# Kernel tuning notes

Hardware: AMD Instinct MI355X
Metric: run time of the kernel (lower is better)

Reference implementation:

```python
import jax, jax.numpy as jnp
import numpy as np

N = 50000          # nodes
H = 202            # hidden = text(200) + selector(2)
E = 100000         # edges per forward edge type
FWD_TYPES = 3      # forward edge types; backward doubles to 6
LAYER_TIMESTEPS = (2,)
POS_MAX = 1024


def _pos_table():
    # transformer-style sinusoidal embeddings for positions [0, POS_MAX)
    inv_freq = 1.0 / (10000.0 ** (jnp.arange(0, H, 2, dtype=jnp.float32) / H))  # [H/2]
    pos = jnp.arange(POS_MAX, dtype=jnp.float32)
    sinusoid = pos[:, None] * inv_freq[None, :]                                  # [POS_MAX, H/2]
    return jnp.concatenate([jnp.sin(sinusoid), jnp.cos(sinusoid)], axis=-1)      # [POS_MAX, H]


def setup_inputs() -> dict:
    key = jax.random.key(0)
    ks = jax.random.split(key, 11)
    L = len(LAYER_TIMESTEPS)
    s = 0.1
    return {
        "node_states": jax.random.normal(ks[0], (N, H), jnp.float32),
        "edge_lists": jax.random.randint(ks[1], (FWD_TYPES, E, 2), 0, N, jnp.int32),
        "pos_lists": jax.random.randint(ks[2], (FWD_TYPES, E), 0, POS_MAX, jnp.int32),
        "msg_W": jax.random.normal(ks[3], (L, H, 2 * FWD_TYPES * H), jnp.float32) * s,
        "msg_b": jax.random.normal(ks[4], (L, 2 * FWD_TYPES * H), jnp.float32) * s,
        "pos_W": jax.random.normal(ks[5], (L, H, H), jnp.float32) * s,
        "pos_b": jax.random.normal(ks[6], (L, H), jnp.float32) * s,
        "gru_Wih": jax.random.normal(ks[7], (L, 3 * H, H), jnp.float32) * s,
        "gru_Whh": jax.random.normal(ks[8], (L, 3 * H, H), jnp.float32) * s,
        "gru_bih": jax.random.normal(ks[9], (L, 3 * H), jnp.float32) * s,
        "gru_bhh": jax.random.normal(ks[10], (L, 3 * H), jnp.float32) * s,
    }


def _ggnn(node_states, src, tgt, pos, divisor,
          msg_W, msg_b, pos_W, pos_b, gru_Wih, gru_Whh, gru_bih, gru_bhh):
    ET = src.shape[0]  # 2 * FWD_TYPES edge types (forward + backward)
    h = node_states
    pos_table = _pos_table()
    for l, steps in enumerate(LAYER_TIMESTEPS):
        # 2*sigmoid(pos_transform(position_embs)) gating, per position id
        gate = 2.0 * jax.nn.sigmoid(pos_table @ pos_W[l] + pos_b[l])  # [POS_MAX, H]
        for _ in range(steps):
            # fused per-edge-type transforms: [N, ET*H] chunked -> [N, ET, H]
            prop = (h @ msg_W[l] + msg_b[l]).reshape(h.shape[0], ET, H)
            messages = jnp.zeros_like(h)
            for i in range(ET):  # small fixed loop over edge types
                m = prop[:, i, :][src[i]] * gate[pos[i]]  # [E, H]
                messages = messages.at[tgt[i]].add(m)
            messages = messages / divisor  # mean aggregation
            # nn.GRUCell(messages, h)
            gi = messages @ gru_Wih[l].T + gru_bih[l]
            gh = h @ gru_Whh[l].T + gru_bhh[l]
            ir, iz, inn = jnp.split(gi, 3, axis=1)
            hr, hz, hn = jnp.split(gh, 3, axis=1)
            r = jax.nn.sigmoid(ir + hr)
            z = jax.nn.sigmoid(iz + hz)
            n = jnp.tanh(inn + r * hn)
            h = (1.0 - z) * n + z * h
    return h


def reference(node_states, edge_lists, pos_lists, msg_W, msg_b, pos_W, pos_b,
              gru_Wih, gru_Whh, gru_bih, gru_bhh):
    # backward edges = flipped forward edges; pos lists duplicated
    src = jnp.concatenate([edge_lists[:, :, 0], edge_lists[:, :, 1]], axis=0)  # [6, E]
    tgt = jnp.concatenate([edge_lists[:, :, 1], edge_lists[:, :, 0]], axis=0)  # [6, E]
    pos = jnp.clip(jnp.concatenate([pos_lists, pos_lists], axis=0), 0, POS_MAX - 1)
    # target bincount over all edge types; zero counts -> 1
    counts = jnp.zeros((node_states.shape[0],), jnp.float32).at[tgt.reshape(-1)].add(1.0)
    divisor = jnp.where(counts == 0, 1.0, counts)[:, None]
    out = _ggnn(node_states, src, tgt, pos, divisor, msg_W, msg_b, pos_W, pos_b,
                gru_Wih, gru_Whh, gru_bih, gru_bhh)
    return out, node_states
```

## Files before the change

### kernel.cpp

```cpp
#include <hip/hip_runtime.h>

#define NN 50000
#define HH 202
#define EE 100000
#define PMX 1024
#define NKT 7
#define PKS2 (16 * NKT * 64 * 8)
#define NEDG (6 * EE)
#define AFR (4 * NKT * 64 * 8)

typedef __attribute__((ext_vector_type(8))) short short8;
typedef __attribute__((ext_vector_type(4))) float v4f;

__device__ __forceinline__ float sigf(float x) { return 1.0f / (1.0f + expf(-x)); }

__device__ __forceinline__ unsigned short f2bf(float x) {
    unsigned int u = __float_as_uint(x);
    unsigned int r = (u + 0x7fffu + ((u >> 16) & 1u)) >> 16;
    return (unsigned short)r;
}
__device__ __forceinline__ float bf2f(unsigned short u) {
    return __uint_as_float(((unsigned int)u) << 16);
}
__device__ __forceinline__ float bflo(unsigned int u) {
    return __uint_as_float(u << 16);
}
__device__ __forceinline__ float bfhi(unsigned int u) {
    return __uint_as_float(u & 0xffff0000u);
}
__device__ __forceinline__ unsigned int bfpack(float lo, float hi) {
    return (unsigned int)f2bf(lo) | ((unsigned int)f2bf(hi) << 16);
}

__global__ void gate_kernel(const float* __restrict__ pos_W, const float* __restrict__ pos_b,
                            unsigned short* __restrict__ gate) {
    int p = blockIdx.x;
    __shared__ float pt[HH];
    int t = threadIdx.x;
    if (t < HH) {
        float v;
        if (t < 101) {
            float invf = expf(-(2.0f * t / 202.0f) * 9.210340371976184f);
            v = sinf((float)p * invf);
        } else {
            int k = t - 101;
            float invf = expf(-(2.0f * k / 202.0f) * 9.210340371976184f);
            v = cosf((float)p * invf);
        }
        pt[t] = v;
    }
    __syncthreads();
    for (int j = t; j < HH; j += blockDim.x) {
        float acc = pos_b[j];
        for (int k = 0; k < HH; ++k) acc += pt[k] * pos_W[k * HH + j];
        gate[p * HH + j] = f2bf(2.0f * sigf(acc));
    }
}

__global__ void pack_kernel(const float* __restrict__ S, int ldb, int row0, int col0, int mode,
                            unsigned short* __restrict__ BP) {
    int idx = blockIdx.x * blockDim.x + threadIdx.x;
    if (idx >= PKS2) return;
    int jj = idx & 7;
    int l = (idx >> 3) & 63;
    int r2 = idx >> 9;
    int cf = r2 / NKT, kt = r2 - cf * NKT;
    int k = kt * 32 + ((l >> 4) << 3) + jj;
    int j = cf * 16 + (l & 15);
    float v = 0.0f;
    if (k < HH && j < HH)
        v = mode ? S[(size_t)(row0 + j) * HH + k] : S[(size_t)k * ldb + col0 + j];
    BP[idx] = f2bf(v);
}

__global__ void count_kernel(const int* __restrict__ el, int* __restrict__ cnt) {
    int idx = blockIdx.x * blockDim.x + threadIdx.x;
    if (idx >= NEDG) return;
    int ty = idx / EE, e = idx - ty * EE;
    int2 pr = (ty < 3) ? reinterpret_cast<const int2*>(el)[ty * EE + e]
                       : reinterpret_cast<const int2*>(el)[(ty - 3) * EE + e];
    int tg = (ty < 3) ? pr.y : pr.x;
    atomicAdd(&cnt[tg], 1);
}

__global__ void scan1_kernel(const int* __restrict__ cnt, int* __restrict__ off,
                             int* __restrict__ bsum) {
    __shared__ int sd[256];
    int t = threadIdx.x, i = blockIdx.x * 256 + t;
    int v = (i < NN) ? cnt[i] : 0;
    sd[t] = v;
    __syncthreads();
    for (int s = 1; s < 256; s <<= 1) {
        int u = (t >= s) ? sd[t - s] : 0;
        __syncthreads();
        sd[t] += u;
        __syncthreads();
    }
    if (i < NN) off[i] = sd[t] - v;
    if (t == 255) bsum[blockIdx.x] = sd[255];
}

__global__ void scan2_kernel(int* __restrict__ bsum, int nb) {
    __shared__ int sd[256];
    int t = threadIdx.x;
    int v = (t < nb) ? bsum[t] : 0;
    sd[t] = v;
    __syncthreads();
    for (int s = 1; s < 256; s <<= 1) {
        int u = (t >= s) ? sd[t - s] : 0;
        __syncthreads();
        sd[t] += u;
        __syncthreads();
    }
    if (t < nb) bsum[t] = sd[t] - v;
}

__global__ void scan3_kernel(int* __restrict__ off, const int* __restrict__ bsum,
                             int* __restrict__ cursor) {
    int i = blockIdx.x * 256 + threadIdx.x;
    if (i < NN) {
        int o = off[i] + bsum[blockIdx.x];
        off[i] = o;
        cursor[i] = o;
    }
    if (i == 0) off[NN] = NEDG;
}

__global__ void inv_kernel(const int* __restrict__ cnt, float* __restrict__ inv) {
    int n = blockIdx.x * blockDim.x + threadIdx.x;
    if (n < NN) inv[n] = 1.0f / (float)max(cnt[n], 1);
}

__global__ void fill_kernel(const int* __restrict__ el, const int* __restrict__ pl,
                            int* __restrict__ cursor, int* __restrict__ edg) {
    int idx = blockIdx.x * blockDim.x + threadIdx.x;
    if (idx >= NEDG) return;
    int ty = idx / EE, e = idx - ty * EE;
    int s, tg;
    if (ty < 3) {
        int2 pr = reinterpret_cast<const int2*>(el)[ty * EE + e];
        s = pr.x; tg = pr.y;
    } else {
        int2 pr = reinterpret_cast<const int2*>(el)[(ty - 3) * EE + e];
        s = pr.y; tg = pr.x;
    }
    int p = pl[(ty % 3) * EE + e];
    p = min(max(p, 0), PMX - 1);
    int slot = atomicAdd(&cursor[tg], 1);
    edg[slot] = (s << 13) | (ty << 10) | p;
}

__device__ __forceinline__ int frag_off(int row, int k) {
    return (((row >> 4) * NKT + (k >> 5)) * 64 + ((k >> 3) & 3) * 16 + (row & 15)) * 8 + (k & 7);
}

__global__ __launch_bounds__(512, 4) void gemm9(
    const void* __restrict__ Asrc, int a_is_f32,
    const unsigned short* __restrict__ BPbase, int npack,
    const float* __restrict__ bias,
    unsigned short* __restrict__ O0, unsigned short* __restrict__ O1, int split) {
    __shared__ alignas(16) unsigned short a_lds[AFR];
    __shared__ alignas(16) unsigned short c_lds[64 * HH];
    const int t = threadIdx.x;
    const int w = t >> 6;
    const int l = t & 63;
    const int lm = l & 15, lh = l >> 4;
    const int rowg = w >> 2, colg = w & 3;
    const int cs = colg * 4;
    const int base = blockIdx.x * 64;
    const int vrows = min(64, NN - base);
    const int nu4 = (vrows * 101) >> 2;

    if (a_is_f32) {
        const float* A = (const float*)Asrc;
        for (int idx = t; idx < 64 * 101; idx += 512) {
            int row = idx / 101;
            int c = idx - row * 101;
            int gn = base + row;
            float2 v = make_float2(0.f, 0.f);
            if (gn < NN) v = *reinterpret_cast<const float2*>(&A[(size_t)gn * HH + c * 2]);
            ushort2 bv; bv.x = f2bf(v.x); bv.y = f2bf(v.y);
            *reinterpret_cast<ushort2*>(&a_lds[frag_off(row, c * 2)]) = bv;
        }
    } else {
        const unsigned short* A = (const unsigned short*)Asrc;
        for (int idx = t; idx < 64 * 101; idx += 512) {
            int row = idx / 101;
            int c = idx - row * 101;
            int gn = base + row;
            ushort2 v; v.x = 0; v.y = 0;
            if (gn < NN) v = *reinterpret_cast<const ushort2*>(&A[(size_t)gn * HH + c * 2]);
            *reinterpret_cast<ushort2*>(&a_lds[frag_off(row, c * 2)]) = v;
        }
    }
    for (int idx = t; idx < 64 * 11; idx += 512) {
        int row = idx / 11;
        int c = idx - row * 11;
        ushort2 z; z.x = 0; z.y = 0;
        *reinterpret_cast<ushort2*>(&a_lds[frag_off(row, HH + c * 2)]) = z;
    }
    __syncthreads();

    const int aoff0 = (rowg * 2) * (NKT * 512) + l * 8;
    const int aoff1 = aoff0 + NKT * 512;

#pragma unroll 1
    for (int p = 0; p < npack; ++p) {
        const unsigned short* BP = BPbase + (size_t)p * PKS2 + (size_t)l * 8;
        const unsigned short* Bs0 = BP + (size_t)(cs + 0) * (NKT * 512);
        const unsigned short* Bs1 = BP + (size_t)(cs + 1) * (NKT * 512);
        const unsigned short* Bs2 = BP + (size_t)(cs + 2) * (NKT * 512);
        const unsigned short* Bs3 = BP + (size_t)(cs + 3) * (NKT * 512);

        v4f acc[4][2];
#pragma unroll
        for (int ci = 0; ci < 4; ++ci) {
            acc[ci][0] = (v4f){0.f, 0.f, 0.f, 0.f};
            acc[ci][1] = (v4f){0.f, 0.f, 0.f, 0.f};
        }

        short8 bA0 = *reinterpret_cast<const short8*>(Bs0);
        short8 bA1 = *reinterpret_cast<const short8*>(Bs1);
        short8 bA2 = *reinterpret_cast<const short8*>(Bs2);
        short8 bA3 = *reinterpret_cast<const short8*>(Bs3);
        short8 bB0 = *reinterpret_cast<const short8*>(Bs0 + 512);
        short8 bB1 = *reinterpret_cast<const short8*>(Bs1 + 512);
        short8 bB2 = *reinterpret_cast<const short8*>(Bs2 + 512);
        short8 bB3 = *reinterpret_cast<const short8*>(Bs3 + 512);
        short8 ac0 = *reinterpret_cast<const short8*>(&a_lds[aoff0]);
        short8 ac1 = *reinterpret_cast<const short8*>(&a_lds[aoff1]);

#pragma unroll
        for (int kt = 0; kt < NKT; ++kt) {
            const int k2 = (kt + 2 <= 6) ? (kt + 2) : 6;
            const int ka2 = k2 * 512;
            short8 bC0 = *reinterpret_cast<const short8*>(Bs0 + ka2);
            short8 bC1 = *reinterpret_cast<const short8*>(Bs1 + ka2);
            short8 bC2 = *reinterpret_cast<const short8*>(Bs2 + ka2);
            short8 bC3 = *reinterpret_cast<const short8*>(Bs3 + ka2);
            const int kn = (kt + 1 <= 6) ? (kt + 1) : 6;
            short8 an0 = *reinterpret_cast<const short8*>(&a_lds[aoff0 + kn * 512]);
            short8 an1 = *reinterpret_cast<const short8*>(&a_lds[aoff1 + kn * 512]);

            acc[0][0] = __builtin_amdgcn_mfma_f32_16x16x32_bf16(ac0, bA0, acc[0][0], 0, 0, 0);
            acc[0][1] = __builtin_amdgcn_mfma_f32_16x16x32_bf16(ac1, bA0, acc[0][1], 0, 0, 0);
            acc[1][0] = __builtin_amdgcn_mfma_f32_16x16x32_bf16(ac0, bA1, acc[1][0], 0, 0, 0);
            acc[1][1] = __builtin_amdgcn_mfma_f32_16x16x32_bf16(ac1, bA1, acc[1][1], 0, 0, 0);
            acc[2][0] = __builtin_amdgcn_mfma_f32_16x16x32_bf16(ac0, bA2, acc[2][0], 0, 0, 0);
            acc[2][1] = __builtin_amdgcn_mfma_f32_16x16x32_bf16(ac1, bA2, acc[2][1], 0, 0, 0);
            acc[3][0] = __builtin_amdgcn_mfma_f32_16x16x32_bf16(ac0, bA3, acc[3][0], 0, 0, 0);
            acc[3][1] = __builtin_amdgcn_mfma_f32_16x16x32_bf16(ac1, bA3, acc[3][1], 0, 0, 0);

            ac0 = an0; ac1 = an1;
            bA0 = bB0; bA1 = bB1; bA2 = bB2; bA3 = bB3;
            bB0 = bC0; bB1 = bC1; bB2 = bC2; bB3 = bC3;
        }

        __syncthreads();
#pragma unroll
        for (int ci = 0; ci < 4; ++ci) {
            int col = (cs + ci) * 16 + lm;
            if (col < HH) {
                float bb = bias ? bias[p * HH + col] : 0.0f;
#pragma unroll
                for (int rfi = 0; rfi < 2; ++rfi) {
#pragma unroll
                    for (int r = 0; r < 4; ++r)
                        c_lds[(rowg * 32 + rfi * 16 + lh * 4 + r) * HH + col] =
                            f2bf(acc[ci][rfi][r] + bb);
                }
            }
        }
        __syncthreads();

        unsigned short* slab = (p < split) ? O0 + (size_t)p * NN * HH
                                           : O1 + (size_t)(p - split) * NN * HH;
        uint4* dst = reinterpret_cast<uint4*>(slab + (size_t)base * HH);
        const uint4* srcp = reinterpret_cast<const uint4*>(c_lds);
        for (int i = t; i < nu4; i += 512) dst[i] = srcp[i];
    }
}

__global__ void agg_kernel(const unsigned short* __restrict__ CH0,
                           const unsigned short* __restrict__ CH45,
                           const int* __restrict__ off, const int* __restrict__ edg,
                           const unsigned short* __restrict__ gate,
                           const float* __restrict__ inv, unsigned short* __restrict__ msgb) {
    int n = blockIdx.x * 4 + (threadIdx.x >> 6);
    if (n >= NN) return;
    int lane = threadIdx.x & 63;
    int s0 = off[n], s1 = off[n + 1];
    const int u1 = 64 + lane;
    const bool u1ok = u1 < 101;
    float a0 = 0.f, a1 = 0.f, a2 = 0.f, a3 = 0.f;
    float b0 = 0.f, b1 = 0.f, b2 = 0.f, b3 = 0.f;
    int i = s0;
    for (; i + 1 < s1; i += 2) {
        int recA = edg[i], recB = edg[i + 1];
        int sA = recA >> 13, tyA = (recA >> 10) & 7, pA = recA & 1023;
        int sB = recB >> 13, tyB = (recB >> 10) & 7, pB = recB & 1023;
        const unsigned int* crA = reinterpret_cast<const unsigned int*>(
            ((tyA < 4) ? CH0 + (size_t)tyA * NN * HH : CH45 + (size_t)(tyA - 4) * NN * HH)
            + (size_t)sA * HH);
        const unsigned int* crB = reinterpret_cast<const unsigned int*>(
            ((tyB < 4) ? CH0 + (size_t)tyB * NN * HH : CH45 + (size_t)(tyB - 4) * NN * HH)
            + (size_t)sB * HH);
        const unsigned int* grA = reinterpret_cast<const unsigned int*>(gate + (size_t)pA * HH);
        const unsigned int* grB = reinterpret_cast<const unsigned int*>(gate + (size_t)pB * HH);
        unsigned int cA0 = crA[lane], gA0 = grA[lane];
        unsigned int cB0 = crB[lane], gB0 = grB[lane];
        a0 += bflo(cA0) * bflo(gA0);
        a1 += bfhi(cA0) * bfhi(gA0);
        b0 += bflo(cB0) * bflo(gB0);
        b1 += bfhi(cB0) * bfhi(gB0);
        if (u1ok) {
            unsigned int cA1 = crA[u1], gA1 = grA[u1];
            unsigned int cB1 = crB[u1], gB1 = grB[u1];
            a2 += bflo(cA1) * bflo(gA1);
            a3 += bfhi(cA1) * bfhi(gA1);
            b2 += bflo(cB1) * bflo(gB1);
            b3 += bfhi(cB1) * bfhi(gB1);
        }
    }
    if (i < s1) {
        int rec = edg[i];
        int src = rec >> 13, ty = (rec >> 10) & 7, p = rec & 1023;
        const unsigned int* cr = reinterpret_cast<const unsigned int*>(
            ((ty < 4) ? CH0 + (size_t)ty * NN * HH : CH45 + (size_t)(ty - 4) * NN * HH)
            + (size_t)src * HH);
        const unsigned int* gr = reinterpret_cast<const unsigned int*>(gate + (size_t)p * HH);
        unsigned int c0 = cr[lane], g0 = gr[lane];
        a0 += bflo(c0) * bflo(g0);
        a1 += bfhi(c0) * bfhi(g0);
        if (u1ok) {
            unsigned int c1 = cr[u1], g1 = gr[u1];
            a2 += bflo(c1) * bflo(g1);
            a3 += bfhi(c1) * bfhi(g1);
        }
    }
    float iv = inv[n];
    unsigned int* mr = reinterpret_cast<unsigned int*>(msgb + (size_t)n * HH);
    mr[lane] = bfpack((a0 + b0) * iv, (a1 + b1) * iv);
    if (u1ok) mr[u1] = bfpack((a2 + b2) * iv, (a3 + b3) * iv);
}

__global__ void gru_ew(float* __restrict__ h, const float* __restrict__ hsrc,
                       const unsigned short* __restrict__ GH,
                       const unsigned short* __restrict__ GIr,
                       const unsigned short* __restrict__ GIzn,
                       const float* __restrict__ bih, const float* __restrict__ bhh) {
    int n = blockIdx.x * 4 + (threadIdx.x >> 6);
    if (n >= NN) return;
    int lane = threadIdx.x & 63;
    const size_t NHu = (size_t)NN * HH / 2;
    const unsigned int* GHu  = reinterpret_cast<const unsigned int*>(GH)  + (size_t)n * 101;
    const unsigned int* GIru = reinterpret_cast<const unsigned int*>(GIr) + (size_t)n * 101;
    const unsigned int* GIzu = reinterpret_cast<const unsigned int*>(GIzn) + (size_t)n * 101;
    const float2* hsp = reinterpret_cast<const float2*>(hsrc + (size_t)n * HH);
    float2* hp = reinterpret_cast<float2*>(h + (size_t)n * HH);
    const float2* bihp = reinterpret_cast<const float2*>(bih);
    const float2* bhhp = reinterpret_cast<const float2*>(bhh);
#pragma unroll
    for (int q = 0; q < 2; ++q) {
        int u = lane + q * 64;
        if (u < 101) {
            unsigned int ghr = GHu[u];
            unsigned int ghz = GHu[NHu + u];
            unsigned int ghn = GHu[2 * NHu + u];
            unsigned int gir = GIru[u];
            unsigned int giz = GIzu[u];
            unsigned int gin = GIzu[NHu + u];
            float2 br = bihp[u], bhr = bhhp[u];
            float2 bz = bihp[101 + u], bhz = bhhp[101 + u];
            float2 bn = bihp[202 + u], bhn = bhhp[202 + u];
            float2 hv = hsp[u];
            float r0 = sigf(bflo(gir) + bflo(ghr) + br.x + bhr.x);
            float r1 = sigf(bfhi(gir) + bfhi(ghr) + br.y + bhr.y);
            float z0 = sigf(bflo(giz) + bflo(ghz) + bz.x + bhz.x);
            float z1 = sigf(bfhi(giz) + bfhi(ghz) + bz.y + bhz.y);
            float n0 = tanhf(bflo(gin) + bn.x + r0 * (bflo(ghn) + bhn.x));
            float n1 = tanhf(bfhi(gin) + bn.y + r1 * (bfhi(ghn) + bhn.y));
            float2 hvo;
            hvo.x = (1.0f - z0) * n0 + z0 * hv.x;
            hvo.y = (1.0f - z1) * n1 + z1 * hv.y;
            hp[u] = hvo;
        }
    }
}

extern "C" void kernel_launch(void* const* d_in, const int* in_sizes, int n_in,
                              void* d_out, int out_size, void* d_ws, size_t ws_size,
                              hipStream_t stream) {
    const float* node_states = (const float*)d_in[0];
    const int*   el          = (const int*)d_in[1];
    const int*   pl          = (const int*)d_in[2];
    const float* msg_W       = (const float*)d_in[3];
    const float* msg_b       = (const float*)d_in[4];
    const float* pos_W       = (const float*)d_in[5];
    const float* pos_b       = (const float*)d_in[6];
    const float* gWih        = (const float*)d_in[7];
    const float* gWhh        = (const float*)d_in[8];
    const float* gbih        = (const float*)d_in[9];
    const float* gbhh        = (const float*)d_in[10];

    float* out  = (float*)d_out;
    float* h    = out;
    float* out2 = out + (size_t)NN * HH;

    unsigned short* CH0  = (unsigned short*)d_ws;
    unsigned short* CH45 = (unsigned short*)out2;
    unsigned short* MSGB = CH0 + (size_t)4 * NN * HH;
    unsigned short* GATE = MSGB + (size_t)NN * HH;
    float* INV  = (float*)(GATE + (size_t)PMX * HH + 8);
    int* CNT    = (int*)(INV + NN);
    int* OFF    = CNT + NN;
    int* CUR    = OFF + NN + 4;
    int* BS     = CUR + NN;
    int* EDG    = BS + 256;
    unsigned short* BPA = (unsigned short*)(EDG + NEDG);
    unsigned short* BPp  = BPA;
    unsigned short* BPih = BPA + (size_t)6 * PKS2;
    unsigned short* BPhh = BPA + (size_t)9 * PKS2;

    const size_t NH = (size_t)NN * HH;
    hipMemsetAsync(CNT, 0, NN * sizeof(int), stream);
    gate_kernel<<<PMX, 256, 0, stream>>>(pos_W, pos_b, GATE);
    const int pkb = (PKS2 + 255) / 256;
    for (int ty = 0; ty < 6; ++ty)
        pack_kernel<<<pkb, 256, 0, stream>>>(msg_W, 1212, 0, ty * HH, 0, BPp + (size_t)ty * PKS2);
    pack_kernel<<<pkb, 256, 0, stream>>>(gWih, 0, 0,   0, 1, BPih);
    pack_kernel<<<pkb, 256, 0, stream>>>(gWih, 0, 202, 0, 1, BPih + PKS2);
    pack_kernel<<<pkb, 256, 0, stream>>>(gWih, 0, 404, 0, 1, BPih + 2 * PKS2);
    pack_kernel<<<pkb, 256, 0, stream>>>(gWhh, 0, 0,   0, 1, BPhh);
    pack_kernel<<<pkb, 256, 0, stream>>>(gWhh, 0, 202, 0, 1, BPhh + PKS2);
    pack_kernel<<<pkb, 256, 0, stream>>>(gWhh, 0, 404, 0, 1, BPhh + 2 * PKS2);

    const int nsb = (NN + 255) / 256;
    count_kernel<<<(NEDG + 255) / 256, 256, 0, stream>>>(el, CNT);
    scan1_kernel<<<nsb, 256, 0, stream>>>(CNT, OFF, BS);
    scan2_kernel<<<1, 256, 0, stream>>>(BS, nsb);
    scan3_kernel<<<nsb, 256, 0, stream>>>(OFF, BS, CUR);
    inv_kernel<<<nsb, 256, 0, stream>>>(CNT, INV);
    fill_kernel<<<(NEDG + 255) / 256, 256, 0, stream>>>(el, pl, CUR, EDG);

    const int gblocks = (NN + 63) / 64;
    const int ewblocks = (NN + 3) / 4;
    for (int step = 0; step < 2; ++step) {
        const float* hsrc = (step == 0) ? node_states : h;
        gemm9<<<gblocks, 512, 0, stream>>>(hsrc, 1, BPp, 6, msg_b, CH0, CH45, 4);
        agg_kernel<<<ewblocks, 256, 0, stream>>>(CH0, CH45, OFF, EDG, GATE, INV, MSGB);
        gemm9<<<gblocks, 512, 0, stream>>>(hsrc, 1, BPhh, 3, nullptr, CH0, nullptr, 4);
        gemm9<<<gblocks, 512, 0, stream>>>(MSGB, 0, BPih, 3, nullptr,
                                           CH0 + 3 * NH, CH45, 1);
        gru_ew<<<ewblocks, 256, 0, stream>>>(h, hsrc, CH0, CH0 + 3 * NH, CH45, gbih, gbhh);
    }
    hipMemcpyAsync(out2, node_states, NH * sizeof(float), hipMemcpyDeviceToDevice, stream);
}
```

Before: 633.0 us.

## Fuse GRU input/hidden GEMMs with summed gates and shrink gemm9 LDS staging

The two separate GRU GEMMs become one kernel, gemmG. It stages both h and the aggregated messages in LDS and accumulates the r and z gate contributions from both weight sets into shared accumulators. It writes only four bf16 slabs with the biases folded in, so gru_ew reads fewer slabs and no bias arrays. gemm9 now stages its output through a half-sized LDS buffer in two passes, drops the register prefetch of B and A fragments, and raises launch bounds to allow more resident blocks. This trades the prefetch pipelining and some extra syncs for higher occupancy and less global traffic.

Measured after the change: 996.5 us. 1.57x slower.

```diff
diff --git a/kernel.cpp b/kernel.cpp
--- a/kernel.cpp
+++ b/kernel.cpp
@@ -154,13 +154,13 @@
     return (((row >> 4) * NKT + (k >> 5)) * 64 + ((k >> 3) & 3) * 16 + (row & 15)) * 8 + (k & 7);
 }
 
-__global__ __launch_bounds__(512, 4) void gemm9(
+__global__ __launch_bounds__(512, 6) void gemm9(
     const void* __restrict__ Asrc, int a_is_f32,
     const unsigned short* __restrict__ BPbase, int npack,
     const float* __restrict__ bias,
     unsigned short* __restrict__ O0, unsigned short* __restrict__ O1, int split) {
     __shared__ alignas(16) unsigned short a_lds[AFR];
-    __shared__ alignas(16) unsigned short c_lds[64 * HH];
+    __shared__ alignas(16) unsigned short c_lds[32 * HH];
     const int t = threadIdx.x;
     const int w = t >> 6;
     const int l = t & 63;
@@ -168,8 +168,6 @@
     const int rowg = w >> 2, colg = w & 3;
     const int cs = colg * 4;
     const int base = blockIdx.x * 64;
-    const int vrows = min(64, NN - base);
-    const int nu4 = (vrows * 101) >> 2;
 
     if (a_is_f32) {
         const float* A = (const float*)Asrc;
@@ -219,65 +217,171 @@
             acc[ci][1] = (v4f){0.f, 0.f, 0.f, 0.f};
         }
 
-        short8 bA0 = *reinterpret_cast<const short8*>(Bs0);
-        short8 bA1 = *reinterpret_cast<const short8*>(Bs1);
-        short8 bA2 = *reinterpret_cast<const short8*>(Bs2);
-        short8 bA3 = *reinterpret_cast<const short8*>(Bs3);
-        short8 bB0 = *reinterpret_cast<const short8*>(Bs0 + 512);
-        short8 bB1 = *reinterpret_cast<const short8*>(Bs1 + 512);
-        short8 bB2 = *reinterpret_cast<const short8*>(Bs2 + 512);
-        short8 bB3 = *reinterpret_cast<const short8*>(Bs3 + 512);
-        short8 ac0 = *reinterpret_cast<const short8*>(&a_lds[aoff0]);
-        short8 ac1 = *reinterpret_cast<const short8*>(&a_lds[aoff1]);
-
 #pragma unroll
         for (int kt = 0; kt < NKT; ++kt) {
-            const int k2 = (kt + 2 <= 6) ? (kt + 2) : 6;
-            const int ka2 = k2 * 512;
-            short8 bC0 = *reinterpret_cast<const short8*>(Bs0 + ka2);
-            short8 bC1 = *reinterpret_cast<const short8*>(Bs1 + ka2);
-            short8 bC2 = *reinterpret_cast<const short8*>(Bs2 + ka2);
-            short8 bC3 = *reinterpret_cast<const short8*>(Bs3 + ka2);
-            const int kn = (kt + 1 <= 6) ? (kt + 1) : 6;
-            short8 an0 = *reinterpret_cast<const short8*>(&a_lds[aoff0 + kn * 512]);
-            short8 an1 = *reinterpret_cast<const short8*>(&a_lds[aoff1 + kn * 512]);
-
-            acc[0][0] = __builtin_amdgcn_mfma_f32_16x16x32_bf16(ac0, bA0, acc[0][0], 0, 0, 0);
-            acc[0][1] = __builtin_amdgcn_mfma_f32_16x16x32_bf16(ac1, bA0, acc[0][1], 0, 0, 0);
-            acc[1][0] = __builtin_amdgcn_mfma_f32_16x16x32_bf16(ac0, bA1, acc[1][0], 0, 0, 0);
-            acc[1][1] = __builtin_amdgcn_mfma_f32_16x16x32_bf16(ac1, bA1, acc[1][1], 0, 0, 0);
-            acc[2][0] = __builtin_amdgcn_mfma_f32_16x16x32_bf16(ac0, bA2, acc[2][0], 0, 0, 0);
-            acc[2][1] = __builtin_amdgcn_mfma_f32_16x16x32_bf16(ac1, bA2, acc[2][1], 0, 0, 0);
-            acc[3][0] = __builtin_amdgcn_mfma_f32_16x16x32_bf16(ac0, bA3, acc[3][0], 0, 0, 0);
-            acc[3][1] = __builtin_amdgcn_mfma_f32_16x16x32_bf16(ac1, bA3, acc[3][1], 0, 0, 0);
-
-            ac0 = an0; ac1 = an1;
-            bA0 = bB0; bA1 = bB1; bA2 = bB2; bA3 = bB3;
-            bB0 = bC0; bB1 = bC1; bB2 = bC2; bB3 = bC3;
-        }
-
-        __syncthreads();
-#pragma unroll
-        for (int ci = 0; ci < 4; ++ci) {
-            int col = (cs + ci) * 16 + lm;
-            if (col < HH) {
-                float bb = bias ? bias[p * HH + col] : 0.0f;
-#pragma unroll
-                for (int rfi = 0; rfi < 2; ++rfi) {
-#pragma unroll
-                    for (int r = 0; r < 4; ++r)
-                        c_lds[(rowg * 32 + rfi * 16 + lh * 4 + r) * HH + col] =
-                            f2bf(acc[ci][rfi][r] + bb);
-                }
-            }
-        }
-        __syncthreads();
+            const int ka = kt * 512;
+            short8 b0 = *reinterpret_cast<const short8*>(Bs0 + ka);
+            short8 b1 = *reinterpret_cast<const short8*>(Bs1 + ka);
+            short8 b2 = *reinterpret_cast<const short8*>(Bs2 + ka);
+            short8 b3 = *reinterpret_cast<const short8*>(Bs3 + ka);
+            short8 a0 = *reinterpret_cast<const short8*>(&a_lds[aoff0 + ka]);
+            short8 a1 = *reinterpret_cast<const short8*>(&a_lds[aoff1 + ka]);
+
+            acc[0][0] = __builtin_amdgcn_mfma_f32_16x16x32_bf16(a0, b0, acc[0][0], 0, 0, 0);
+            acc[0][1] = __builtin_amdgcn_mfma_f32_16x16x32_bf16(a1, b0, acc[0][1], 0, 0, 0);
+            acc[1][0] = __builtin_amdgcn_mfma_f32_16x16x32_bf16(a0, b1, acc[1][0], 0, 0, 0);
+            acc[1][1] = __builtin_amdgcn_mfma_f32_16x16x32_bf16(a1, b1, acc[1][1], 0, 0, 0);
+            acc[2][0] = __builtin_amdgcn_mfma_f32_16x16x32_bf16(a0, b2, acc[2][0], 0, 0, 0);
+            acc[2][1] = __builtin_amdgcn_mfma_f32_16x16x32_bf16(a1, b2, acc[2][1], 0, 0, 0);
+            acc[3][0] = __builtin_amdgcn_mfma_f32_16x16x32_bf16(a0, b3, acc[3][0], 0, 0, 0);
+            acc[3][1] = __builtin_amdgcn_mfma_f32_16x16x32_bf16(a1, b3, acc[3][1], 0, 0, 0);
+        }
 
         unsigned short* slab = (p < split) ? O0 + (size_t)p * NN * HH
                                            : O1 + (size_t)(p - split) * NN * HH;
-        uint4* dst = reinterpret_cast<uint4*>(slab + (size_t)base * HH);
-        const uint4* srcp = reinterpret_cast<const uint4*>(c_lds);
-        for (int i = t; i < nu4; i += 512) dst[i] = srcp[i];
+#pragma unroll 1
+        for (int rfi = 0; rfi < 2; ++rfi) {
+            __syncthreads();
+#pragma unroll
+            for (int ci = 0; ci < 4; ++ci) {
+                int col = (cs + ci) * 16 + lm;
+                if (col < HH) {
+                    float bb = bias ? bias[p * HH + col] : 0.0f;
+#pragma unroll
+                    for (int r = 0; r < 4; ++r)
+                        c_lds[(rowg * 16 + lh * 4 + r) * HH + col] = f2bf(acc[ci][rfi][r] + bb);
+                }
+            }
+            __syncthreads();
+            int r0 = base + rfi * 16;
+            int r1 = base + 32 + rfi * 16;
+            const uint4* s = reinterpret_cast<const uint4*>(c_lds);
+            if (r0 + 16 <= NN) {
+                uint4* d0 = reinterpret_cast<uint4*>(slab + (size_t)r0 * HH);
+                for (int i = t; i < 404; i += 512) d0[i] = s[i];
+            }
+            if (r1 + 16 <= NN) {
+                uint4* d1 = reinterpret_cast<uint4*>(slab + (size_t)r1 * HH);
+                for (int i = t; i < 404; i += 512) d1[i] = s[404 + i];
+            }
+        }
+    }
+}
+
+__global__ __launch_bounds__(512, 4) void gemmG(
+    const float* __restrict__ hsrc, const unsigned short* __restrict__ msgb,
+    const unsigned short* __restrict__ BPih, const unsigned short* __restrict__ BPhh,
+    const float* __restrict__ bih, const float* __restrict__ bhh,
+    unsigned short* __restrict__ O) {
+    __shared__ alignas(16) unsigned short a_lds[2 * AFR];
+    __shared__ alignas(16) unsigned short c_lds[32 * HH];
+    const int t = threadIdx.x;
+    const int w = t >> 6;
+    const int l = t & 63;
+    const int lm = l & 15, lh = l >> 4;
+    const int rowg = w >> 2, colg = w & 3;
+    const int cs = colg * 4;
+    const int base = blockIdx.x * 64;
+
+    for (int idx = t; idx < 64 * 101; idx += 512) {
+        int row = idx / 101;
+        int c = idx - row * 101;
+        int gn = base + row;
+        float2 v = make_float2(0.f, 0.f);
+        ushort2 m; m.x = 0; m.y = 0;
+        if (gn < NN) {
+            v = *reinterpret_cast<const float2*>(&hsrc[(size_t)gn * HH + c * 2]);
+            m = *reinterpret_cast<const ushort2*>(&msgb[(size_t)gn * HH + c * 2]);
+        }
+        ushort2 bv; bv.x = f2bf(v.x); bv.y = f2bf(v.y);
+        int fo = frag_off(row, c * 2);
+        *reinterpret_cast<ushort2*>(&a_lds[fo]) = bv;
+        *reinterpret_cast<ushort2*>(&a_lds[AFR + fo]) = m;
+    }
+    for (int idx = t; idx < 64 * 11; idx += 512) {
+        int row = idx / 11;
+        int c = idx - row * 11;
+        ushort2 z; z.x = 0; z.y = 0;
+        int fo = frag_off(row, HH + c * 2);
+        *reinterpret_cast<ushort2*>(&a_lds[fo]) = z;
+        *reinterpret_cast<ushort2*>(&a_lds[AFR + fo]) = z;
+    }
+    __syncthreads();
+
+    const int aoffh = (rowg * 2) * (NKT * 512) + l * 8;
+    const int aoffm = AFR + aoffh;
+
+#pragma unroll 1
+    for (int p = 0; p < 4; ++p) {
+        const bool useH = (p != 3);
+        const bool useM = (p != 2);
+        const int bsel = (p < 2) ? p : 2;
+        const unsigned short* Bh = BPhh + (size_t)bsel * PKS2 + (size_t)l * 8;
+        const unsigned short* Bm = BPih + (size_t)bsel * PKS2 + (size_t)l * 8;
+
+        v4f acc[4][2];
+#pragma unroll
+        for (int ci = 0; ci < 4; ++ci) {
+            acc[ci][0] = (v4f){0.f, 0.f, 0.f, 0.f};
+            acc[ci][1] = (v4f){0.f, 0.f, 0.f, 0.f};
+        }
+
+#pragma unroll 1
+        for (int kt = 0; kt < NKT; ++kt) {
+            const int ka = kt * 512;
+            if (useH) {
+                short8 a0 = *reinterpret_cast<const short8*>(&a_lds[aoffh + ka]);
+                short8 a1 = *reinterpret_cast<const short8*>(&a_lds[aoffh + NKT * 512 + ka]);
+#pragma unroll
+                for (int ci = 0; ci < 4; ++ci) {
+                    short8 b = *reinterpret_cast<const short8*>(
+                        Bh + (size_t)(cs + ci) * (NKT * 512) + ka);
+                    acc[ci][0] = __builtin_amdgcn_mfma_f32_16x16x32_bf16(a0, b, acc[ci][0], 0, 0, 0);
+                    acc[ci][1] = __builtin_amdgcn_mfma_f32_16x16x32_bf16(a1, b, acc[ci][1], 0, 0, 0);
+                }
+            }
+            if (useM) {
+                short8 a0 = *reinterpret_cast<const short8*>(&a_lds[aoffm + ka]);
+                short8 a1 = *reinterpret_cast<const short8*>(&a_lds[aoffm + NKT * 512 + ka]);
+#pragma unroll
+                for (int ci = 0; ci < 4; ++ci) {
+                    short8 b = *reinterpret_cast<const short8*>(
+                        Bm + (size_t)(cs + ci) * (NKT * 512) + ka);
+                    acc[ci][0] = __builtin_amdgcn_mfma_f32_16x16x32_bf16(a0, b, acc[ci][0], 0, 0, 0);
+                    acc[ci][1] = __builtin_amdgcn_mfma_f32_16x16x32_bf16(a1, b, acc[ci][1], 0, 0, 0);
+                }
+            }
+        }
+
+        unsigned short* slab = O + (size_t)p * NN * HH;
+#pragma unroll 1
+        for (int rfi = 0; rfi < 2; ++rfi) {
+            __syncthreads();
+#pragma unroll
+            for (int ci = 0; ci < 4; ++ci) {
+                int col = (cs + ci) * 16 + lm;
+                if (col < HH) {
+                    float bb = (p == 0) ? (bih[col] + bhh[col])
+                             : (p == 1) ? (bih[202 + col] + bhh[202 + col])
+                             : (p == 2) ? bhh[404 + col] : bih[404 + col];
+#pragma unroll
+                    for (int r = 0; r < 4; ++r)
+                        c_lds[(rowg * 16 + lh * 4 + r) * HH + col] = f2bf(acc[ci][rfi][r] + bb);
+                }
+            }
+            __syncthreads();
+            int r0 = base + rfi * 16;
+            int r1 = base + 32 + rfi * 16;
+            const uint4* s = reinterpret_cast<const uint4*>(c_lds);
+            if (r0 + 16 <= NN) {
+                uint4* d0 = reinterpret_cast<uint4*>(slab + (size_t)r0 * HH);
+                for (int i = t; i < 404; i += 512) d0[i] = s[i];
+            }
+            if (r1 + 16 <= NN) {
+                uint4* d1 = reinterpret_cast<uint4*>(slab + (size_t)r1 * HH);
+                for (int i = t; i < 404; i += 512) d1[i] = s[404 + i];
+            }
+        }
     }
 }
 
@@ -345,41 +449,29 @@
 }
 
 __global__ void gru_ew(float* __restrict__ h, const float* __restrict__ hsrc,
-                       const unsigned short* __restrict__ GH,
-                       const unsigned short* __restrict__ GIr,
-                       const unsigned short* __restrict__ GIzn,
-                       const float* __restrict__ bih, const float* __restrict__ bhh) {
+                       const unsigned short* __restrict__ G) {
     int n = blockIdx.x * 4 + (threadIdx.x >> 6);
     if (n >= NN) return;
     int lane = threadIdx.x & 63;
     const size_t NHu = (size_t)NN * HH / 2;
-    const unsigned int* GHu  = reinterpret_cast<const unsigned int*>(GH)  + (size_t)n * 101;
-    const unsigned int* GIru = reinterpret_cast<const unsigned int*>(GIr) + (size_t)n * 101;
-    const unsigned int* GIzu = reinterpret_cast<const unsigned int*>(GIzn) + (size_t)n * 101;
+    const unsigned int* Gu = reinterpret_cast<const unsigned int*>(G) + (size_t)n * 101;
     const float2* hsp = reinterpret_cast<const float2*>(hsrc + (size_t)n * HH);
     float2* hp = reinterpret_cast<float2*>(h + (size_t)n * HH);
-    const float2* bihp = reinterpret_cast<const float2*>(bih);
-    const float2* bhhp = reinterpret_cast<const float2*>(bhh);
 #pragma unroll
     for (int q = 0; q < 2; ++q) {
         int u = lane + q * 64;
         if (u < 101) {
-            unsigned int ghr = GHu[u];
-            unsigned int ghz = GHu[NHu + u];
-            unsigned int ghn = GHu[2 * NHu + u];
-            unsigned int gir = GIru[u];
-            unsigned int giz = GIzu[u];
-            unsigned int gin = GIzu[NHu + u];
-            float2 br = bihp[u], bhr = bhhp[u];
-            float2 bz = bihp[101 + u], bhz = bhhp[101 + u];
-            float2 bn = bihp[202 + u], bhn = bhhp[202 + u];
+            unsigned int sr = Gu[u];
+            unsigned int sz = Gu[NHu + u];
+            unsigned int hn = Gu[2 * NHu + u];
+            unsigned int in_ = Gu[3 * NHu + u];
             float2 hv = hsp[u];
-            float r0 = sigf(bflo(gir) + bflo(ghr) + br.x + bhr.x);
-            float r1 = sigf(bfhi(gir) + bfhi(ghr) + br.y + bhr.y);
-            float z0 = sigf(bflo(giz) + bflo(ghz) + bz.x + bhz.x);
-            float z1 = sigf(bfhi(giz) + bfhi(ghz) + bz.y + bhz.y);
-            float n0 = tanhf(bflo(gin) + bn.x + r0 * (bflo(ghn) + bhn.x));
-            float n1 = tanhf(bfhi(gin) + bn.y + r1 * (bfhi(ghn) + bhn.y));
+            float r0 = sigf(bflo(sr));
+            float r1 = sigf(bfhi(sr));
+            float z0 = sigf(bflo(sz));
+            float z1 = sigf(bfhi(sz));
+            float n0 = tanhf(bflo(in_) + r0 * bflo(hn));
+            float n1 = tanhf(bfhi(in_) + r1 * bfhi(hn));
             float2 hvo;
             hvo.x = (1.0f - z0) * n0 + z0 * hv.x;
             hvo.y = (1.0f - z1) * n1 + z1 * hv.y;
@@ -449,10 +541,8 @@
         const float* hsrc = (step == 0) ? node_states : h;
         gemm9<<<gblocks, 512, 0, stream>>>(hsrc, 1, BPp, 6, msg_b, CH0, CH45, 4);
         agg_kernel<<<ewblocks, 256, 0, stream>>>(CH0, CH45, OFF, EDG, GATE, INV, MSGB);
-        gemm9<<<gblocks, 512, 0, stream>>>(hsrc, 1, BPhh, 3, nullptr, CH0, nullptr, 4);
-        gemm9<<<gblocks, 512, 0, stream>>>(MSGB, 0, BPih, 3, nullptr,
-                                           CH0 + 3 * NH, CH45, 1);
-        gru_ew<<<ewblocks, 256, 0, stream>>>(h, hsrc, CH0, CH0 + 3 * NH, CH45, gbih, gbhh);
+        gemmG<<<gblocks, 512, 0, stream>>>(hsrc, MSGB, BPih, BPhh, gbih, gbhh, CH0);
+        gru_ew<<<ewblocks, 256, 0, stream>>>(h, hsrc, CH0);
     }
     hipMemcpyAsync(out2, node_states, NH * sizeof(float), hipMemcpyDeviceToDevice, stream);
 }
```
